# Kernel optimization log

Measured on AMD Instinct MI355X. Metric: run time of the kernel, lower is better.

The kernel has to match this reference:

```python
import jax, jax.numpy as jnp
import numpy as np

D_MODEL = 1024
NUM_HEADS = 16
HEAD_DIM = D_MODEL // NUM_HEADS
B, S = 2, 2048


def setup_inputs() -> dict:
    key = jax.random.key(0)
    ks = jax.random.split(key, 12)
    s = 0.02
    inp = {
        "Q": jax.random.normal(ks[0], (B, S, D_MODEL), jnp.float32),
        "K": jax.random.normal(ks[1], (B, S, D_MODEL), jnp.float32),
        "V": jax.random.normal(ks[2], (B, S, D_MODEL), jnp.float32),
        # causal mask: 1 = keep, 0 = masked (matches masked_fill(mask == 0, -inf))
        "mask": jnp.tril(jnp.ones((S, S), jnp.int32))[None, None, :, :],
        "Wq": jax.random.normal(ks[3], (D_MODEL, D_MODEL), jnp.float32) * s,
        "bq": jnp.zeros((D_MODEL,), jnp.float32),
        "Wk": jax.random.normal(ks[4], (D_MODEL, D_MODEL), jnp.float32) * s,
        "bk": jnp.zeros((D_MODEL,), jnp.float32),
        "Wv": jax.random.normal(ks[5], (D_MODEL, D_MODEL), jnp.float32) * s,
        "bv": jnp.zeros((D_MODEL,), jnp.float32),
        "Wo": jax.random.normal(ks[6], (D_MODEL, D_MODEL), jnp.float32) * s,
        "bo": jnp.zeros((D_MODEL,), jnp.float32),
    }
    return inp


def reference(Q, K, V, mask, Wq, bq, Wk, bk, Wv, bv, Wo, bo):
    b, sq, _ = Q.shape
    sk = K.shape[1]
    # linear projections (torch Linear: x @ W^T + b)
    q = Q @ Wq.T + bq
    k = K @ Wk.T + bk
    v = V @ Wv.T + bv
    # [B, H, S, Dh]
    q = q.reshape(b, sq, NUM_HEADS, HEAD_DIM).transpose(0, 2, 1, 3)
    k = k.reshape(b, sk, NUM_HEADS, HEAD_DIM).transpose(0, 2, 1, 3)
    v = v.reshape(b, sk, NUM_HEADS, HEAD_DIM).transpose(0, 2, 1, 3)
    scores = jnp.einsum("bhqd,bhkd->bhqk", q, k) / jnp.sqrt(
        jnp.asarray(HEAD_DIM, q.dtype)
    )
    scores = jnp.where(mask == 0, jnp.asarray(-jnp.inf, scores.dtype), scores)
    attn = jax.nn.softmax(scores, axis=-1)
    out = jnp.einsum("bhqk,bhkd->bhqd", attn, v)
    out = out.transpose(0, 2, 1, 3).reshape(b, sq, D_MODEL)
    return out @ Wo.T + bo
```

## Files before the change

kernel.cpp:

```cpp
#include <hip/hip_runtime.h>
#include <hip/hip_bf16.h>
#include <cstdint>
#include <cstddef>


typedef __attribute__((ext_vector_type(8))) short bf16x8;
typedef __attribute__((ext_vector_type(4))) short bf16x4;
typedef __attribute__((ext_vector_type(4))) float f32x4;
typedef __attribute__((ext_vector_type(2))) unsigned int u32x2;

constexpr int GM = 4096;
constexpr int GN = 1024;
constexpr int GK = 1024;
#define QSCALE 0.18033688011112042f

#if __has_builtin(__builtin_amdgcn_mfma_f32_16x16x16bf16_1k)
#define MFMA16(a, b, c) __builtin_amdgcn_mfma_f32_16x16x16bf16_1k((a), (b), (c), 0, 0, 0)
#elif __has_builtin(__builtin_amdgcn_mfma_f32_16x16x16_bf16)
#define MFMA16(a, b, c) __builtin_amdgcn_mfma_f32_16x16x16_bf16((a), (b), (c), 0, 0, 0)
#else
static __device__ __forceinline__ f32x4 mfma16_asm(bf16x4 a, bf16x4 b, f32x4 c) {
  asm volatile("v_mfma_f32_16x16x16_bf16 %0, %1, %2, %0" : "+v"(c) : "v"(a), "v"(b));
  return c;
}
#define MFMA16(a, b, c) mfma16_asm((a), (b), (c))
#endif

#if __has_builtin(__builtin_amdgcn_exp2f)
#define EXP2(x) __builtin_amdgcn_exp2f(x)
#else
#define EXP2(x) exp2f(x)
#endif

__device__ __forceinline__ void gload_lds16(const __hip_bfloat16* g, __hip_bfloat16* l) {
  __builtin_amdgcn_global_load_lds(
      (const __attribute__((address_space(1))) void*)g,
      (__attribute__((address_space(3))) void*)l, 16, 0, 0);
}

__device__ __forceinline__ unsigned lds_off(const void* p) {
  return (unsigned)(uintptr_t)(__attribute__((address_space(3))) const void*)p;
}

__device__ __forceinline__ void cvt8(const float* in, __hip_bfloat16* out, int i) {
  const float4* p = (const float4*)in;
  float4 a = p[i * 2];
  float4 c = p[i * 2 + 1];
  union { __hip_bfloat16 h[8]; bf16x8 v; } u;
  u.h[0] = __float2bfloat16(a.x); u.h[1] = __float2bfloat16(a.y);
  u.h[2] = __float2bfloat16(a.z); u.h[3] = __float2bfloat16(a.w);
  u.h[4] = __float2bfloat16(c.x); u.h[5] = __float2bfloat16(c.y);
  u.h[6] = __float2bfloat16(c.z); u.h[7] = __float2bfloat16(c.w);
  *(bf16x8*)(out + (size_t)i * 8) = u.v;
}

__global__ __launch_bounds__(256) void cvt3_kernel(
    const float* __restrict__ a0, const float* __restrict__ a1,
    const float* __restrict__ a2, __hip_bfloat16* __restrict__ o0,
    __hip_bfloat16* __restrict__ o1, __hip_bfloat16* __restrict__ o2, int n8) {
  int i = blockIdx.x * 256 + threadIdx.x;
  if (i >= n8) return;
  const int z = blockIdx.z;
  const float* in = (z == 0) ? a0 : (z == 1) ? a1 : a2;
  __hip_bfloat16* out = (z == 0) ? o0 : (z == 1) ? o1 : o2;
  cvt8(in, out, i);
}

__global__ __launch_bounds__(256) void cvt4_kernel(
    const float* __restrict__ a0, const float* __restrict__ a1,
    const float* __restrict__ a2, const float* __restrict__ a3,
    __hip_bfloat16* __restrict__ o0, __hip_bfloat16* __restrict__ o1,
    __hip_bfloat16* __restrict__ o2, __hip_bfloat16* __restrict__ o3, int n8) {
  int i = blockIdx.x * 256 + threadIdx.x;
  if (i >= n8) return;
  const int z = blockIdx.z;
  const float* in = (z == 0) ? a0 : (z == 1) ? a1 : (z == 2) ? a2 : a3;
  __hip_bfloat16* out = (z == 0) ? o0 : (z == 1) ? o1 : (z == 2) ? o2 : o3;
  cvt8(in, out, i);
}

__global__ __launch_bounds__(256) void qkv_gemm_kernel(
    const __hip_bfloat16* __restrict__ Xq, const __hip_bfloat16* __restrict__ Xk,
    const __hip_bfloat16* __restrict__ Xv,
    const __hip_bfloat16* __restrict__ Wq, const __hip_bfloat16* __restrict__ Wk,
    const __hip_bfloat16* __restrict__ Wv,
    const float* __restrict__ bq, const float* __restrict__ bk,
    const float* __restrict__ bv,
    __hip_bfloat16* __restrict__ oq, __hip_bfloat16* __restrict__ ok,
    __hip_bfloat16* __restrict__ ov) {
  __shared__ __align__(16) __hip_bfloat16 Asm[128 * 32];
  __shared__ __align__(16) __hip_bfloat16 Bsm[128 * 32];
  const int tid = threadIdx.x;
  const int l = tid & 63, w = tid >> 6;
  const int lo = l & 15, hi = l >> 4;
  const int wr = w >> 1, wc = w & 1;
  const int widx = blockIdx.x >> 3;
  const int n0 = (blockIdx.x & 7) * 128;
  const int m0 = blockIdx.y * 128;
  const int srow = (l >> 2), scol = (l & 3) * 8;

  const __hip_bfloat16* A  = (widx == 0) ? Xq : (widx == 1) ? Xk : Xv;
  const __hip_bfloat16* Bw = (widx == 0) ? Wq : (widx == 1) ? Wk : Wv;
  const float* bias        = (widx == 0) ? bq : (widx == 1) ? bk : bv;
  __hip_bfloat16* C        = (widx == 0) ? oq : (widx == 1) ? ok : ov;
  const float oscale       = (widx == 0) ? QSCALE : 1.0f;

  f32x4 acc[4][4] = {};

  for (int kt = 0; kt < GK; kt += 32) {
#pragma unroll
    for (int i = 0; i < 2; ++i) {
      const int c = i * 4 + w;
      const int row = c * 16 + srow;
      gload_lds16(A + (size_t)(m0 + row) * GK + kt + scol, &Asm[c * 512]);
      gload_lds16(Bw + (size_t)(n0 + row) * GK + kt + scol, &Bsm[c * 512]);
    }
    __syncthreads();
    bf16x8 af[4], bfr[4];
#pragma unroll
    for (int f = 0; f < 4; ++f) {
      af[f]  = *(const bf16x8*)&Asm[(wr * 64 + f * 16 + lo) * 32 + hi * 8];
      bfr[f] = *(const bf16x8*)&Bsm[(wc * 64 + f * 16 + lo) * 32 + hi * 8];
    }
#pragma unroll
    for (int i = 0; i < 4; ++i)
#pragma unroll
      for (int j = 0; j < 4; ++j)
        acc[i][j] = __builtin_amdgcn_mfma_f32_16x16x32_bf16(af[i], bfr[j], acc[i][j], 0, 0, 0);
    __syncthreads();
  }

#pragma unroll
  for (int i = 0; i < 4; ++i) {
#pragma unroll
    for (int j = 0; j < 4; ++j) {
      const int gc = n0 + wc * 64 + j * 16 + lo;
      const float bs = bias[gc];
#pragma unroll
      for (int r = 0; r < 4; ++r) {
        const int gr = m0 + wr * 64 + i * 16 + hi * 4 + r;
        C[(size_t)gr * GN + gc] = __float2bfloat16((acc[i][j][r] + bs) * oscale);
      }
    }
  }
}

__global__ __launch_bounds__(256) void gemm_out_kernel(
    const __hip_bfloat16* __restrict__ A,
    const __hip_bfloat16* __restrict__ Bw,
    const float* __restrict__ bias, float* __restrict__ C) {
  __shared__ __align__(16) __hip_bfloat16 Asm[64 * 32];
  __shared__ __align__(16) __hip_bfloat16 Bsm[128 * 32];
  const int tid = threadIdx.x;
  const int l = tid & 63, w = tid >> 6;
  const int lo = l & 15, hi = l >> 4;
  const int wr = w >> 1, wc = w & 1;
  const int m0 = blockIdx.y * 64, n0 = blockIdx.x * 128;
  const int srowA = (l >> 2), scol = (l & 3) * 8;

  f32x4 acc[2][4] = {};

  for (int kt = 0; kt < GK; kt += 32) {
    {
      const int rowA = w * 16 + srowA;
      gload_lds16(A + (size_t)(m0 + rowA) * GK + kt + scol, &Asm[w * 512]);
    }
#pragma unroll
    for (int i = 0; i < 2; ++i) {
      const int c = i * 4 + w;
      const int row = c * 16 + srowA;
      gload_lds16(Bw + (size_t)(n0 + row) * GK + kt + scol, &Bsm[c * 512]);
    }
    __syncthreads();
    bf16x8 af[2], bfr[4];
#pragma unroll
    for (int f = 0; f < 2; ++f)
      af[f] = *(const bf16x8*)&Asm[(wr * 32 + f * 16 + lo) * 32 + hi * 8];
#pragma unroll
    for (int f = 0; f < 4; ++f)
      bfr[f] = *(const bf16x8*)&Bsm[(wc * 64 + f * 16 + lo) * 32 + hi * 8];
#pragma unroll
    for (int i = 0; i < 2; ++i)
#pragma unroll
      for (int j = 0; j < 4; ++j)
        acc[i][j] = __builtin_amdgcn_mfma_f32_16x16x32_bf16(af[i], bfr[j], acc[i][j], 0, 0, 0);
    __syncthreads();
  }

#pragma unroll
  for (int i = 0; i < 2; ++i) {
#pragma unroll
    for (int j = 0; j < 4; ++j) {
      const int gc = n0 + wc * 64 + j * 16 + lo;
      const float bs = bias[gc];
#pragma unroll
      for (int r = 0; r < 4; ++r) {
        const int gr = m0 + wr * 32 + i * 16 + hi * 4 + r;
        C[(size_t)gr * GN + gc] = acc[i][j][r] + bs;
      }
    }
  }
}

__global__ __launch_bounds__(512) void attn_kernel(
    const __hip_bfloat16* __restrict__ qb,
    const __hip_bfloat16* __restrict__ kb,
    const __hip_bfloat16* __restrict__ vb,
    __hip_bfloat16* __restrict__ ob) {
  __shared__ __align__(16) __hip_bfloat16 Kl[64 * 64];
  __shared__ __align__(16) __hip_bfloat16 Vl[16 * 528];

  const int tid = threadIdx.x;
  const int l = tid & 63, w = tid >> 6;
  const int lo = l & 15, hi = l >> 4;
  const int bid = blockIdx.x;
  const int qt = 15 - (bid & 15);
  const int h = (bid >> 4) & 15;
  const int b = bid >> 8;
  const int q0 = qt * 128;

  const size_t base = (size_t)b * 2048 * 1024 + (size_t)h * 64;
  const __hip_bfloat16* qp = qb + base;
  const __hip_bfloat16* kp = kb + base;
  const __hip_bfloat16* vp = vb + base;
  __hip_bfloat16* op = ob + base;

  const int qrow = q0 + w * 16 + lo;
  bf16x8 qa[2];
  qa[0] = *(const bf16x8*)(qp + (size_t)qrow * 1024 + hi * 8);
  qa[1] = *(const bf16x8*)(qp + (size_t)qrow * 1024 + 32 + hi * 8);

  f32x4 accO[4] = {};
  float lsum = 0.f;

  const int vrow = tid >> 3;
  const int vd0 = (tid & 7) * 8;
  const int vsub = (vrow >> 4) * 4 + (vd0 >> 4);
  const int vpos = (vrow & 15) * 16 + (vd0 & 15);
  const int krow = w * 8 + (l >> 3);
  const int kcolb = ((l & 7) * 16) ^ ((krow & 7) << 4);

  const unsigned vtr_base = lds_off(&Vl[0]) + (unsigned)l * 8;

  bf16x8 vr = *(const bf16x8*)(vp + (size_t)vrow * 1024 + vd0);

  const int nfull = 2 * qt;
  const int nsteps = nfull + 2;

  auto step = [&](int t, int mode) {
    const int kv0 = t * 64;
    __syncthreads();
    *(bf16x8*)&Vl[vsub * 528 + vpos] = vr;
    gload_lds16(kp + (size_t)(kv0 + krow) * 1024 + (kcolb >> 1), &Kl[w * 512]);
    __syncthreads();
    if (t + 1 < nsteps)
      vr = *(const bf16x8*)(vp + (size_t)(kv0 + 64 + vrow) * 1024 + vd0);
    if (mode == 2) return;

    f32x4 sf[4];
#pragma unroll
    for (int f = 0; f < 4; ++f) {
      f32x4 s = {};
#pragma unroll
      for (int ks = 0; ks < 2; ++ks) {
        const int rl = f * 16 + lo;
        const int colb = (ks * 64 + hi * 16) ^ ((rl & 7) << 4);
        const bf16x8 kf = *(const bf16x8*)((const char*)&Kl[0] + rl * 128 + colb);
        s = __builtin_amdgcn_mfma_f32_16x16x32_bf16(kf, qa[ks], s, 0, 0, 0);
      }
      sf[f] = s;
    }

    const int qi = q0 + w * 16 + lo;
    bf16x4 pf[4];
#pragma unroll
    for (int f = 0; f < 4; ++f) {
      float p[4];
#pragma unroll
      for (int r = 0; r < 4; ++r) {
        if (mode == 1) {
          const int kvi = kv0 + f * 16 + hi * 4 + r;
          p[r] = (kvi <= qi) ? EXP2(sf[f][r]) : 0.f;
        } else {
          p[r] = EXP2(sf[f][r]);
        }
        lsum += p[r];
      }
      union { __hip_bfloat16 hh[4]; bf16x4 v; } u;
      u.hh[0] = __float2bfloat16(p[0]);
      u.hh[1] = __float2bfloat16(p[1]);
      u.hh[2] = __float2bfloat16(p[2]);
      u.hh[3] = __float2bfloat16(p[3]);
      pf[f] = u.v;
    }

    u32x2 vv[4][4];
#pragma unroll
    for (int tc = 0; tc < 4; ++tc)
#pragma unroll
      for (int fc = 0; fc < 4; ++fc) {
        const unsigned addr = vtr_base + (unsigned)((tc * 4 + fc) * 1056);
        asm volatile("ds_read_b64_tr_b16 %0, %1" : "=v"(vv[tc][fc]) : "v"(addr));
      }
    asm volatile("s_waitcnt lgkmcnt(0)" ::: "memory");
    __builtin_amdgcn_sched_barrier(0);
#pragma unroll
    for (int tc = 0; tc < 4; ++tc) {
#pragma unroll
      for (int fc = 0; fc < 4; ++fc) {
        union { u32x2 u2; bf16x4 v; } cv;
        cv.u2 = vv[tc][fc];
        accO[fc] = MFMA16(pf[tc], cv.v, accO[fc]);
      }
    }
  };

  for (int t = 0; t < nfull; ++t) step(t, 0);
  step(nfull, (w < 4) ? 1 : 0);
  step(nfull + 1, (w < 4) ? 2 : 1);

  lsum += __shfl_xor(lsum, 16);
  lsum += __shfl_xor(lsum, 32);
#pragma unroll
  for (int r = 0; r < 4; ++r) {
    const float lr = __shfl(lsum, hi * 4 + r);
    const float inv = 1.f / lr;
    const int qg = q0 + w * 16 + hi * 4 + r;
#pragma unroll
    for (int fc = 0; fc < 4; ++fc)
      op[(size_t)qg * 1024 + fc * 16 + lo] = __float2bfloat16(accO[fc][r] * inv);
  }
}

extern "C" void kernel_launch(void* const* d_in, const int* in_sizes, int n_in,
                              void* d_out, int out_size, void* d_ws, size_t ws_size,
                              hipStream_t stream) {
  const float* Q  = (const float*)d_in[0];
  const float* K  = (const float*)d_in[1];
  const float* V  = (const float*)d_in[2];
  const float* Wq = (const float*)d_in[4];
  const float* bq = (const float*)d_in[5];
  const float* Wk = (const float*)d_in[6];
  const float* bk = (const float*)d_in[7];
  const float* Wv = (const float*)d_in[8];
  const float* bv = (const float*)d_in[9];
  const float* Wo = (const float*)d_in[10];
  const float* bo = (const float*)d_in[11];
  float* out = (float*)d_out;

  uint8_t* ws = (uint8_t*)d_ws;
  const size_t MB = 1024 * 1024;
  __hip_bfloat16* Qb   = (__hip_bfloat16*)(ws + 0 * MB);
  __hip_bfloat16* Kb   = (__hip_bfloat16*)(ws + 8 * MB);
  __hip_bfloat16* Vb   = (__hip_bfloat16*)(ws + 16 * MB);
  __hip_bfloat16* Wqb  = (__hip_bfloat16*)(ws + 24 * MB);
  __hip_bfloat16* Wkb  = (__hip_bfloat16*)(ws + 26 * MB);
  __hip_bfloat16* Wvb  = (__hip_bfloat16*)(ws + 28 * MB);
  __hip_bfloat16* Wob  = (__hip_bfloat16*)(ws + 30 * MB);
  __hip_bfloat16* qbuf = (__hip_bfloat16*)(ws + 32 * MB);
  __hip_bfloat16* kbuf = (__hip_bfloat16*)(ws + 40 * MB);
  __hip_bfloat16* vbuf = (__hip_bfloat16*)(ws + 48 * MB);
  __hip_bfloat16* abuf = (__hip_bfloat16*)(ws + 56 * MB);

  cvt3_kernel<<<dim3(2048, 1, 3), 256, 0, stream>>>(Q, K, V, Qb, Kb, Vb, 524288);
  cvt4_kernel<<<dim3(512, 1, 4), 256, 0, stream>>>(Wq, Wk, Wv, Wo, Wqb, Wkb, Wvb, Wob, 131072);

  qkv_gemm_kernel<<<dim3(24, 32), 256, 0, stream>>>(
      Qb, Kb, Vb, Wqb, Wkb, Wvb, bq, bk, bv, qbuf, kbuf, vbuf);

  attn_kernel<<<2 * 16 * 16, 512, 0, stream>>>(qbuf, kbuf, vbuf, abuf);

  gemm_out_kernel<<<dim3(8, 64), 256, 0, stream>>>(abuf, Wob, bo, out);
}
```

Before: 238.8 us.

## Double-buffer K/V tiles in attention, interleave causal tiles, merge convert kernels

The attention kernel now double-buffers the K and V shared-memory tiles. The next tile's stores and async loads are issued before the current tile's compute, which cuts the two barriers per step down to one. Block-to-query-tile order is reversed for the second batch so long and short causal tiles interleave. The two fp32-to-bf16 convert launches are merged into one seven-way launch whose weight slices exit early. This doubles attention LDS use, which may lower occupancy.

```diff
diff --git a/kernel.cpp b/kernel.cpp
--- a/kernel.cpp
+++ b/kernel.cpp
@@ -42,7 +42,30 @@
   return (unsigned)(uintptr_t)(__attribute__((address_space(3))) const void*)p;
 }
 
-__device__ __forceinline__ void cvt8(const float* in, __hip_bfloat16* out, int i) {
+__global__ __launch_bounds__(256) void cvt7_kernel(
+    const float* __restrict__ a0, const float* __restrict__ a1,
+    const float* __restrict__ a2, const float* __restrict__ a3,
+    const float* __restrict__ a4, const float* __restrict__ a5,
+    const float* __restrict__ a6,
+    __hip_bfloat16* __restrict__ o0, __hip_bfloat16* __restrict__ o1,
+    __hip_bfloat16* __restrict__ o2, __hip_bfloat16* __restrict__ o3,
+    __hip_bfloat16* __restrict__ o4, __hip_bfloat16* __restrict__ o5,
+    __hip_bfloat16* __restrict__ o6) {
+  const int z = blockIdx.z;
+  const int n8 = (z < 3) ? 524288 : 131072;
+  int i = blockIdx.x * 256 + threadIdx.x;
+  if (i >= n8) return;
+  const float* in;
+  __hip_bfloat16* out;
+  switch (z) {
+    case 0: in = a0; out = o0; break;
+    case 1: in = a1; out = o1; break;
+    case 2: in = a2; out = o2; break;
+    case 3: in = a3; out = o3; break;
+    case 4: in = a4; out = o4; break;
+    case 5: in = a5; out = o5; break;
+    default: in = a6; out = o6; break;
+  }
   const float4* p = (const float4*)in;
   float4 a = p[i * 2];
   float4 c = p[i * 2 + 1];
@@ -52,31 +75,6 @@
   u.h[4] = __float2bfloat16(c.x); u.h[5] = __float2bfloat16(c.y);
   u.h[6] = __float2bfloat16(c.z); u.h[7] = __float2bfloat16(c.w);
   *(bf16x8*)(out + (size_t)i * 8) = u.v;
-}
-
-__global__ __launch_bounds__(256) void cvt3_kernel(
-    const float* __restrict__ a0, const float* __restrict__ a1,
-    const float* __restrict__ a2, __hip_bfloat16* __restrict__ o0,
-    __hip_bfloat16* __restrict__ o1, __hip_bfloat16* __restrict__ o2, int n8) {
-  int i = blockIdx.x * 256 + threadIdx.x;
-  if (i >= n8) return;
-  const int z = blockIdx.z;
-  const float* in = (z == 0) ? a0 : (z == 1) ? a1 : a2;
-  __hip_bfloat16* out = (z == 0) ? o0 : (z == 1) ? o1 : o2;
-  cvt8(in, out, i);
-}
-
-__global__ __launch_bounds__(256) void cvt4_kernel(
-    const float* __restrict__ a0, const float* __restrict__ a1,
-    const float* __restrict__ a2, const float* __restrict__ a3,
-    __hip_bfloat16* __restrict__ o0, __hip_bfloat16* __restrict__ o1,
-    __hip_bfloat16* __restrict__ o2, __hip_bfloat16* __restrict__ o3, int n8) {
-  int i = blockIdx.x * 256 + threadIdx.x;
-  if (i >= n8) return;
-  const int z = blockIdx.z;
-  const float* in = (z == 0) ? a0 : (z == 1) ? a1 : (z == 2) ? a2 : a3;
-  __hip_bfloat16* out = (z == 0) ? o0 : (z == 1) ? o1 : (z == 2) ? o2 : o3;
-  cvt8(in, out, i);
 }
 
 __global__ __launch_bounds__(256) void qkv_gemm_kernel(
@@ -207,16 +205,17 @@
     const __hip_bfloat16* __restrict__ kb,
     const __hip_bfloat16* __restrict__ vb,
     __hip_bfloat16* __restrict__ ob) {
-  __shared__ __align__(16) __hip_bfloat16 Kl[64 * 64];
-  __shared__ __align__(16) __hip_bfloat16 Vl[16 * 528];
+  __shared__ __align__(16) __hip_bfloat16 Kl[2][64 * 64];
+  __shared__ __align__(16) __hip_bfloat16 Vl[2][16 * 528];
 
   const int tid = threadIdx.x;
   const int l = tid & 63, w = tid >> 6;
   const int lo = l & 15, hi = l >> 4;
   const int bid = blockIdx.x;
-  const int qt = 15 - (bid & 15);
+  const int kk = bid & 15;
   const int h = (bid >> 4) & 15;
   const int b = bid >> 8;
+  const int qt = b ? (15 - kk) : kk;
   const int q0 = qt * 128;
 
   const size_t base = (size_t)b * 2048 * 1024 + (size_t)h * 64;
@@ -235,86 +234,98 @@
 
   const int vrow = tid >> 3;
   const int vd0 = (tid & 7) * 8;
-  const int vsub = (vrow >> 4) * 4 + (vd0 >> 4);
-  const int vpos = (vrow & 15) * 16 + (vd0 & 15);
+  const int vidx = ((vrow >> 4) * 4 + (vd0 >> 4)) * 528 + (vrow & 15) * 16 + (vd0 & 15);
   const int krow = w * 8 + (l >> 3);
   const int kcolb = ((l & 7) * 16) ^ ((krow & 7) << 4);
 
-  const unsigned vtr_base = lds_off(&Vl[0]) + (unsigned)l * 8;
+  const unsigned vtr0 = lds_off(&Vl[0][0]) + (unsigned)l * 8;
+  const unsigned vtr1 = lds_off(&Vl[1][0]) + (unsigned)l * 8;
+
+  const int nsteps = 2 * qt + 2;
 
   bf16x8 vr = *(const bf16x8*)(vp + (size_t)vrow * 1024 + vd0);
-
-  const int nfull = 2 * qt;
-  const int nsteps = nfull + 2;
+  gload_lds16(kp + (size_t)krow * 1024 + (kcolb >> 1), &Kl[0][w * 512]);
+  *(bf16x8*)&Vl[0][vidx] = vr;
+  vr = *(const bf16x8*)(vp + (size_t)(64 + vrow) * 1024 + vd0);
+  __syncthreads();
+
+  int c = 0;
 
   auto step = [&](int t, int mode) {
     const int kv0 = t * 64;
-    __syncthreads();
-    *(bf16x8*)&Vl[vsub * 528 + vpos] = vr;
-    gload_lds16(kp + (size_t)(kv0 + krow) * 1024 + (kcolb >> 1), &Kl[w * 512]);
-    __syncthreads();
-    if (t + 1 < nsteps)
-      vr = *(const bf16x8*)(vp + (size_t)(kv0 + 64 + vrow) * 1024 + vd0);
-    if (mode == 2) return;
-
-    f32x4 sf[4];
-#pragma unroll
-    for (int f = 0; f < 4; ++f) {
-      f32x4 s = {};
-#pragma unroll
-      for (int ks = 0; ks < 2; ++ks) {
-        const int rl = f * 16 + lo;
-        const int colb = (ks * 64 + hi * 16) ^ ((rl & 7) << 4);
-        const bf16x8 kf = *(const bf16x8*)((const char*)&Kl[0] + rl * 128 + colb);
-        s = __builtin_amdgcn_mfma_f32_16x16x32_bf16(kf, qa[ks], s, 0, 0, 0);
-      }
-      sf[f] = s;
-    }
-
-    const int qi = q0 + w * 16 + lo;
-    bf16x4 pf[4];
-#pragma unroll
-    for (int f = 0; f < 4; ++f) {
-      float p[4];
-#pragma unroll
-      for (int r = 0; r < 4; ++r) {
-        if (mode == 1) {
-          const int kvi = kv0 + f * 16 + hi * 4 + r;
-          p[r] = (kvi <= qi) ? EXP2(sf[f][r]) : 0.f;
-        } else {
-          p[r] = EXP2(sf[f][r]);
+    if (t + 1 < nsteps) {
+      *(bf16x8*)&Vl[c ^ 1][vidx] = vr;
+      gload_lds16(kp + (size_t)(kv0 + 64 + krow) * 1024 + (kcolb >> 1),
+                  &Kl[c ^ 1][w * 512]);
+    }
+    if (t + 2 < nsteps)
+      vr = *(const bf16x8*)(vp + (size_t)(kv0 + 128 + vrow) * 1024 + vd0);
+
+    if (mode != 2) {
+      const char* klbase = (const char*)&Kl[c][0];
+      f32x4 sf[4];
+#pragma unroll
+      for (int f = 0; f < 4; ++f) {
+        f32x4 s = {};
+#pragma unroll
+        for (int ks = 0; ks < 2; ++ks) {
+          const int rl = f * 16 + lo;
+          const int colb = (ks * 64 + hi * 16) ^ ((rl & 7) << 4);
+          const bf16x8 kf = *(const bf16x8*)(klbase + rl * 128 + colb);
+          s = __builtin_amdgcn_mfma_f32_16x16x32_bf16(kf, qa[ks], s, 0, 0, 0);
         }
-        lsum += p[r];
-      }
-      union { __hip_bfloat16 hh[4]; bf16x4 v; } u;
-      u.hh[0] = __float2bfloat16(p[0]);
-      u.hh[1] = __float2bfloat16(p[1]);
-      u.hh[2] = __float2bfloat16(p[2]);
-      u.hh[3] = __float2bfloat16(p[3]);
-      pf[f] = u.v;
-    }
-
-    u32x2 vv[4][4];
-#pragma unroll
-    for (int tc = 0; tc < 4; ++tc)
-#pragma unroll
-      for (int fc = 0; fc < 4; ++fc) {
-        const unsigned addr = vtr_base + (unsigned)((tc * 4 + fc) * 1056);
-        asm volatile("ds_read_b64_tr_b16 %0, %1" : "=v"(vv[tc][fc]) : "v"(addr));
-      }
-    asm volatile("s_waitcnt lgkmcnt(0)" ::: "memory");
-    __builtin_amdgcn_sched_barrier(0);
-#pragma unroll
-    for (int tc = 0; tc < 4; ++tc) {
-#pragma unroll
-      for (int fc = 0; fc < 4; ++fc) {
-        union { u32x2 u2; bf16x4 v; } cv;
-        cv.u2 = vv[tc][fc];
-        accO[fc] = MFMA16(pf[tc], cv.v, accO[fc]);
-      }
-    }
+        sf[f] = s;
+      }
+
+      const int qi = q0 + w * 16 + lo;
+      bf16x4 pf[4];
+#pragma unroll
+      for (int f = 0; f < 4; ++f) {
+        float p[4];
+#pragma unroll
+        for (int r = 0; r < 4; ++r) {
+          if (mode == 1) {
+            const int kvi = kv0 + f * 16 + hi * 4 + r;
+            p[r] = (kvi <= qi) ? EXP2(sf[f][r]) : 0.f;
+          } else {
+            p[r] = EXP2(sf[f][r]);
+          }
+          lsum += p[r];
+        }
+        union { __hip_bfloat16 hh[4]; bf16x4 v; } u;
+        u.hh[0] = __float2bfloat16(p[0]);
+        u.hh[1] = __float2bfloat16(p[1]);
+        u.hh[2] = __float2bfloat16(p[2]);
+        u.hh[3] = __float2bfloat16(p[3]);
+        pf[f] = u.v;
+      }
+
+      const unsigned vtr = c ? vtr1 : vtr0;
+      u32x2 vv[4][4];
+#pragma unroll
+      for (int tc = 0; tc < 4; ++tc)
+#pragma unroll
+        for (int fc = 0; fc < 4; ++fc) {
+          const unsigned addr = vtr + (unsigned)((tc * 4 + fc) * 1056);
+          asm volatile("ds_read_b64_tr_b16 %0, %1" : "=v"(vv[tc][fc]) : "v"(addr));
+        }
+      asm volatile("s_waitcnt lgkmcnt(0)" ::: "memory");
+      __builtin_amdgcn_sched_barrier(0);
+#pragma unroll
+      for (int tc = 0; tc < 4; ++tc) {
+#pragma unroll
+        for (int fc = 0; fc < 4; ++fc) {
+          union { u32x2 u2; bf16x4 v; } cv;
+          cv.u2 = vv[tc][fc];
+          accO[fc] = MFMA16(pf[tc], cv.v, accO[fc]);
+        }
+      }
+    }
+    __syncthreads();
+    c ^= 1;
   };
 
+  const int nfull = 2 * qt;
   for (int t = 0; t < nfull; ++t) step(t, 0);
   step(nfull, (w < 4) ? 1 : 0);
   step(nfull + 1, (w < 4) ? 2 : 1);
@@ -362,8 +373,8 @@
   __hip_bfloat16* vbuf = (__hip_bfloat16*)(ws + 48 * MB);
   __hip_bfloat16* abuf = (__hip_bfloat16*)(ws + 56 * MB);
 
-  cvt3_kernel<<<dim3(2048, 1, 3), 256, 0, stream>>>(Q, K, V, Qb, Kb, Vb, 524288);
-  cvt4_kernel<<<dim3(512, 1, 4), 256, 0, stream>>>(Wq, Wk, Wv, Wo, Wqb, Wkb, Wvb, Wob, 131072);
+  cvt7_kernel<<<dim3(2048, 1, 7), 256, 0, stream>>>(
+      Q, K, V, Wq, Wk, Wv, Wo, Qb, Kb, Vb, Wqb, Wkb, Wvb, Wob);
 
   qkv_gemm_kernel<<<dim3(24, 32), 256, 0, stream>>>(
       Qb, Kb, Vb, Wqb, Wkb, Wvb, bq, bk, bv, qbuf, kbuf, vbuf);
```

After: 225.9 us. 1.06x faster.
